# Performance work log

Hardware: AMD Instinct MI355X
Metric: run time of the kernel (lower is better)

The kernel has to match this reference:

```python
import jax, jax.numpy as jnp
import numpy as np

BN_EPSILON = 1e-05


def hard_sigmoid(x):
    return jnp.clip((x + 1.0) / 2.0, 0.0, 1.0)


def setup_inputs() -> dict:
    key = jax.random.key(0)
    kx, kw, kb = jax.random.split(key, 3)
    # NHWC activations
    x = jax.random.normal(kx, (64, 112, 112, 64), dtype=jnp.float32)
    # HWIO kernel initialized ~ truncated_normal(stddev=0.2), then Bernoulli-binarized
    # to +/-1 once at graph-construction time (set_input_shape), so we sample here.
    k_init = 0.2 * jax.random.normal(kw, (3, 3, 64, 64), dtype=jnp.float32)
    kernels = 2.0 * jax.random.bernoulli(kb, hard_sigmoid(k_init)).astype(jnp.float32) - 1.0
    # tf.contrib.layers.batch_norm defaults: center=True (beta), scale=False (no gamma)
    beta = jnp.zeros((64,), dtype=jnp.float32)
    return {"x": x, "kernels": kernels, "beta": beta}


def reference(x, kernels, beta):
    # Training-mode batch norm: per-batch moments over (N, H, W)
    mean = jnp.mean(x, axis=(0, 1, 2))
    var = jnp.var(x, axis=(0, 1, 2))
    x_bn = (x - mean) * jax.lax.rsqrt(var + BN_EPSILON) + beta
    # NOTE: original code computes conv(sign(x_bn), k) but immediately overwrites it
    # with conv(x_bn, k); the effective forward uses the batch-normed (non-signed)
    # activations with the binarized (+/-1) kernels.
    a = jax.lax.conv_general_dilated(
        x_bn, kernels,
        window_strides=(1, 1),
        padding="SAME",
        dimension_numbers=("NHWC", "HWIO", "NHWC"),
    )
    return a
```

## Files before the change

kernel.cpp:

```cpp
#include <hip/hip_runtime.h>

typedef __attribute__((ext_vector_type(8))) short bf16x8;
typedef __attribute__((ext_vector_type(8))) unsigned short u16x8;
typedef __attribute__((ext_vector_type(4))) float f32x4;

#define HW      112
#define CH      64
#define PIX_IMG (HW*HW)
#define N4TOT   (64*112*112*64/4)
#define NPIX_F  802816.0f

#define WS_HV_BYTE  1280
#define WS_W_BYTE   4096
#define WS_XBF_BYTE (4u<<20)

__device__ __forceinline__ unsigned short f2bf(float f) {
  unsigned u = __float_as_uint(f);
  u += 0x7FFFu + ((u >> 16) & 1u);
  return (unsigned short)(u >> 16);
}

__global__ void zero_ws(float* __restrict__ ws) {
  ws[threadIdx.x] = 0.0f;
}

template <bool WRITE_BF>
__global__ __launch_bounds__(256) void stats_kernel(const float* __restrict__ x,
                                                    float* __restrict__ ws,
                                                    unsigned short* __restrict__ xbf) {
  __shared__ float red[128];
  const int tid = threadIdx.x;
  if (tid < 128) red[tid] = 0.0f;
  __syncthreads();

  const float4* __restrict__ x4 = (const float4*)x;
  float4 s = make_float4(0.f, 0.f, 0.f, 0.f);
  float4 q = make_float4(0.f, 0.f, 0.f, 0.f);
  const int stride = gridDim.x * 256;
  #pragma unroll 4
  for (int i = blockIdx.x * 256 + tid; i < N4TOT; i += stride) {
    float4 v = x4[i];
    s.x += v.x; s.y += v.y; s.z += v.z; s.w += v.w;
    q.x = fmaf(v.x, v.x, q.x); q.y = fmaf(v.y, v.y, q.y);
    q.z = fmaf(v.z, v.z, q.z); q.w = fmaf(v.w, v.w, q.w);
    if (WRITE_BF) {
      ushort4 o;
      o.x = f2bf(v.x); o.y = f2bf(v.y); o.z = f2bf(v.z); o.w = f2bf(v.w);
      *(ushort4*)(xbf + 4 * i) = o;
    }
  }
  #pragma unroll
  for (int m = 16; m <= 32; m <<= 1) {
    s.x += __shfl_xor(s.x, m); s.y += __shfl_xor(s.y, m);
    s.z += __shfl_xor(s.z, m); s.w += __shfl_xor(s.w, m);
    q.x += __shfl_xor(q.x, m); q.y += __shfl_xor(q.y, m);
    q.z += __shfl_xor(q.z, m); q.w += __shfl_xor(q.w, m);
  }
  if ((tid & 63) < 16) {
    const int c0 = (tid & 15) * 4;
    atomicAdd(&red[c0 + 0], s.x); atomicAdd(&red[c0 + 1], s.y);
    atomicAdd(&red[c0 + 2], s.z); atomicAdd(&red[c0 + 3], s.w);
    atomicAdd(&red[64 + c0 + 0], q.x); atomicAdd(&red[64 + c0 + 1], q.y);
    atomicAdd(&red[64 + c0 + 2], q.z); atomicAdd(&red[64 + c0 + 3], q.w);
  }
  __syncthreads();
  if (tid < 128) atomicAdd(&ws[tid], red[tid]);
}

__global__ __launch_bounds__(256) void finalize_kernel(const float* __restrict__ beta,
                                                       const float* __restrict__ k,
                                                       float* __restrict__ ws) {
  __shared__ float sb[64];
  __shared__ float part[256];
  const int tid = threadIdx.x;
  if (tid < 64) {
    float mean = ws[tid] * (1.0f / NPIX_F);
    float var  = fmaxf(ws[64 + tid] * (1.0f / NPIX_F) - mean * mean, 0.0f);
    float sc = rsqrtf(var + 1e-5f);
    float b  = beta[tid] - mean * sc;
    ws[128 + tid] = sc;
    ws[192 + tid] = b;
    ((unsigned short*)((char*)ws + WS_HV_BYTE))[tid] = f2bf(-b / sc);
    sb[tid] = b;
  }
  __syncthreads();
  const int co = tid & 63, pt = tid >> 6;
  float a = 0.f;
  #pragma unroll 8
  for (int t = pt; t < 576; t += 4)
    a = fmaf(sb[t & 63], k[t * 64 + co], a);
  part[tid] = a;
  __syncthreads();
  if (tid < 64)
    ws[256 + tid] = part[tid] + part[64 + tid] + part[128 + tid] + part[192 + tid];
}

__global__ __launch_bounds__(256) void prep_w(const float* __restrict__ k,
                                              const float* __restrict__ ws,
                                              unsigned short* __restrict__ wsw) {
  const int oidx = blockIdx.x * 256 + threadIdx.x;
  const int j  = oidx & 7;
  const int co = (oidx >> 3) & 63;
  const int qd = (oidx >> 9) & 3;
  const int t2 = oidx >> 11;
  const int tap = t2 % 9;
  const int h   = t2 / 9;
  const int ci  = h * 32 + qd * 8 + j;
  wsw[oidx] = f2bf(k[(tap * 64 + ci) * 64 + co] * ws[128 + ci]);
}

template <bool USE_BF>
__global__ __launch_bounds__(448, 4) void conv_kernel(const float* __restrict__ x,
                                                      const unsigned short* __restrict__ xbf,
                                                      const unsigned short* __restrict__ wsw,
                                                      const float* __restrict__ ws,
                                                      float* __restrict__ out) {
  __shared__ unsigned short Xs[6 * 114 * 40];
  __shared__ unsigned short Wd[2 * 6144];
  const int tid = threadIdx.x;
  const int bid = blockIdx.x;
  const int n  = bid / 28;
  const int h0 = (bid % 28) * 4;

  const int lane = tid & 63;
  const int wv   = tid >> 6;
  const int qd   = lane >> 4;
  const int cc   = lane & 15;
  const int wvb  = wv * 16;

  const unsigned short* hv = (const unsigned short*)((const char*)ws + WS_HV_BYTE);

  f32x4 acc[4][4];
  {
    const float* bo = ws + 256;
    #pragma unroll
    for (int mt = 0; mt < 4; ++mt) {
      const f32x4 bv = *(const f32x4*)(bo + mt * 16 + qd * 4);
      #pragma unroll
      for (int r = 0; r < 4; ++r) acc[r][mt] = bv;
    }
  }

  for (int half = 0; half < 2; ++half) {
    {
      u16x8 hv8[4];
      #pragma unroll
      for (int o = 0; o < 4; ++o) hv8[o] = *(const u16x8*)(hv + half * 32 + o * 8);
      for (int c = tid; c < 2736; c += 448) {
        const int o  = c & 3;
        const int pi = c >> 2;
        const int p  = pi % 114;
        const int r  = pi / 114;
        const int w  = p - 1;
        const int g  = h0 + r - 1;
        u16x8 v;
        if ((unsigned)w < 112u && (unsigned)g < 112u) {
          const int base = ((n * 112 + g) * 112 + w) * 64 + half * 32 + o * 8;
          if (USE_BF) {
            v = *(const u16x8*)(xbf + base);
          } else {
            const float* sp = x + base;
            const float4 a = *(const float4*)sp;
            const float4 b = *(const float4*)(sp + 4);
            v = (u16x8){f2bf(a.x), f2bf(a.y), f2bf(a.z), f2bf(a.w),
                        f2bf(b.x), f2bf(b.y), f2bf(b.z), f2bf(b.w)};
          }
        } else {
          v = hv8[o];
        }
        *(u16x8*)(&Xs[pi * 40 + o * 8]) = v;
      }
    }
    const unsigned short* wh = wsw + half * 18432;
    for (int t = tid; t < 768; t += 448)
      *(u16x8*)(&Wd[t * 8]) = *(const u16x8*)(wh + t * 8);
    __syncthreads();

    for (int dh = 0; dh < 3; ++dh) {
      if (dh < 2) {
        const unsigned short* ws_src = wh + (dh + 1) * 6144;
        const int nb = ((dh + 1) & 1) * 6144;
        for (int t = tid; t < 768; t += 448)
          *(u16x8*)(&Wd[nb + t * 8]) = *(const u16x8*)(ws_src + t * 8);
      }
      const int cb = (dh & 1) * 6144;
      #pragma unroll
      for (int dw = 0; dw < 3; ++dw) {
        bf16x8 xb[4];
        #pragma unroll
        for (int r = 0; r < 4; ++r)
          xb[r] = *(const bf16x8*)(&Xs[((r + dh) * 114 + wvb + dw + cc) * 40 + qd * 8]);
        #pragma unroll
        for (int mt = 0; mt < 4; ++mt) {
          const bf16x8 wa = *(const bf16x8*)(&Wd[cb + ((dw * 4 + qd) * 64 + mt * 16 + cc) * 8]);
          #pragma unroll
          for (int r = 0; r < 4; ++r)
            acc[r][mt] = __builtin_amdgcn_mfma_f32_16x16x32_bf16(wa, xb[r], acc[r][mt], 0, 0, 0);
        }
      }
      __syncthreads();
    }
  }

  #pragma unroll
  for (int r = 0; r < 4; ++r) {
    const int pix = n * PIX_IMG + (h0 + r) * 112 + wvb + cc;
    float* op = out + pix * 64 + qd * 4;
    #pragma unroll
    for (int mt = 0; mt < 4; ++mt)
      *(f32x4*)(op + mt * 16) = acc[r][mt];
  }
}

extern "C" void kernel_launch(void* const* d_in, const int* in_sizes, int n_in,
                              void* d_out, int out_size, void* d_ws, size_t ws_size,
                              hipStream_t stream) {
  const float* x    = (const float*)d_in[0];
  const float* kern = (const float*)d_in[1];
  const float* beta = (const float*)d_in[2];
  float* out = (float*)d_out;
  float* ws  = (float*)d_ws;
  unsigned short* wsw = (unsigned short*)((char*)d_ws + WS_W_BYTE);
  unsigned short* xbf = (unsigned short*)((char*)d_ws + WS_XBF_BYTE);

  const bool use_bf = ws_size >= (size_t)WS_XBF_BYTE + 102760448ull;

  zero_ws<<<1, 128, 0, stream>>>(ws);
  if (use_bf) stats_kernel<true ><<<1024, 256, 0, stream>>>(x, ws, xbf);
  else        stats_kernel<false><<<1024, 256, 0, stream>>>(x, ws, xbf);
  finalize_kernel<<<1, 256, 0, stream>>>(beta, kern, ws);
  prep_w<<<144, 256, 0, stream>>>(kern, ws, wsw);
  if (use_bf) conv_kernel<true ><<<64 * 28, 448, 0, stream>>>(x, xbf, wsw, ws, out);
  else        conv_kernel<false><<<64 * 28, 448, 0, stream>>>(x, xbf, wsw, ws, out);
}
```

Measured before the change: 485.5 us.

## Restructure conv staging: full-weight LDS, reordered tap loops, block swizzle, nontemporal IO

The conv kernel now loads all nine taps of weights for a half into LDS at once, removing per-row weight double-buffering and two barriers per half. It swaps the loop order to dw-outer/dh-inner with a rotating register window of input rows, which cuts LDS reads. It changes the Xs layout to channel-quad-major and remaps block ids so consecutive blocks spread across XCDs. The stats kernel and output stores now use nontemporal loads and stores. LDS usage grows (about 36KB for weights plus the input tile), which could limit occupancy, and the bf16 staging written nontemporally may not stay cached for the conv pass.

```diff
diff --git a/kernel.cpp b/kernel.cpp
--- a/kernel.cpp
+++ b/kernel.cpp
@@ -2,6 +2,7 @@
 
 typedef __attribute__((ext_vector_type(8))) short bf16x8;
 typedef __attribute__((ext_vector_type(8))) unsigned short u16x8;
+typedef __attribute__((ext_vector_type(4))) unsigned short u16x4;
 typedef __attribute__((ext_vector_type(4))) float f32x4;
 
 #define HW      112
@@ -33,35 +34,35 @@
   if (tid < 128) red[tid] = 0.0f;
   __syncthreads();
 
-  const float4* __restrict__ x4 = (const float4*)x;
-  float4 s = make_float4(0.f, 0.f, 0.f, 0.f);
-  float4 q = make_float4(0.f, 0.f, 0.f, 0.f);
+  const f32x4* __restrict__ x4 = (const f32x4*)x;
+  f32x4 s = {0.f, 0.f, 0.f, 0.f};
+  f32x4 q = {0.f, 0.f, 0.f, 0.f};
   const int stride = gridDim.x * 256;
   #pragma unroll 4
   for (int i = blockIdx.x * 256 + tid; i < N4TOT; i += stride) {
-    float4 v = x4[i];
-    s.x += v.x; s.y += v.y; s.z += v.z; s.w += v.w;
-    q.x = fmaf(v.x, v.x, q.x); q.y = fmaf(v.y, v.y, q.y);
-    q.z = fmaf(v.z, v.z, q.z); q.w = fmaf(v.w, v.w, q.w);
+    f32x4 v = __builtin_nontemporal_load(&x4[i]);
+    s += v;
+    q += v * v;
     if (WRITE_BF) {
-      ushort4 o;
-      o.x = f2bf(v.x); o.y = f2bf(v.y); o.z = f2bf(v.z); o.w = f2bf(v.w);
-      *(ushort4*)(xbf + 4 * i) = o;
+      u16x4 o = {f2bf(v[0]), f2bf(v[1]), f2bf(v[2]), f2bf(v[3])};
+      __builtin_nontemporal_store(o, (u16x4*)(xbf + 4 * i));
     }
   }
   #pragma unroll
   for (int m = 16; m <= 32; m <<= 1) {
-    s.x += __shfl_xor(s.x, m); s.y += __shfl_xor(s.y, m);
-    s.z += __shfl_xor(s.z, m); s.w += __shfl_xor(s.w, m);
-    q.x += __shfl_xor(q.x, m); q.y += __shfl_xor(q.y, m);
-    q.z += __shfl_xor(q.z, m); q.w += __shfl_xor(q.w, m);
+    #pragma unroll
+    for (int j = 0; j < 4; ++j) {
+      s[j] += __shfl_xor(s[j], m);
+      q[j] += __shfl_xor(q[j], m);
+    }
   }
   if ((tid & 63) < 16) {
     const int c0 = (tid & 15) * 4;
-    atomicAdd(&red[c0 + 0], s.x); atomicAdd(&red[c0 + 1], s.y);
-    atomicAdd(&red[c0 + 2], s.z); atomicAdd(&red[c0 + 3], s.w);
-    atomicAdd(&red[64 + c0 + 0], q.x); atomicAdd(&red[64 + c0 + 1], q.y);
-    atomicAdd(&red[64 + c0 + 2], q.z); atomicAdd(&red[64 + c0 + 3], q.w);
+    #pragma unroll
+    for (int j = 0; j < 4; ++j) {
+      atomicAdd(&red[c0 + j], s[j]);
+      atomicAdd(&red[64 + c0 + j], q[j]);
+    }
   }
   __syncthreads();
   if (tid < 128) atomicAdd(&ws[tid], red[tid]);
@@ -115,10 +116,11 @@
                                                       const unsigned short* __restrict__ wsw,
                                                       const float* __restrict__ ws,
                                                       float* __restrict__ out) {
-  __shared__ unsigned short Xs[6 * 114 * 40];
-  __shared__ unsigned short Wd[2 * 6144];
+  __shared__ unsigned short Xs[4 * 6 * 114 * 8];
+  __shared__ unsigned short Wd[2304 * 8];
   const int tid = threadIdx.x;
-  const int bid = blockIdx.x;
+  int bid = (int)blockIdx.x;
+  bid = (bid & 7) * 224 + (bid >> 3);
   const int n  = bid / 28;
   const int h0 = (bid % 28) * 4;
 
@@ -146,7 +148,7 @@
       u16x8 hv8[4];
       #pragma unroll
       for (int o = 0; o < 4; ++o) hv8[o] = *(const u16x8*)(hv + half * 32 + o * 8);
-      for (int c = tid; c < 2736; c += 448) {
+      auto stage = [&](int c) {
         const int o  = c & 3;
         const int pi = c >> 2;
         const int p  = pi % 114;
@@ -160,46 +162,54 @@
             v = *(const u16x8*)(xbf + base);
           } else {
             const float* sp = x + base;
-            const float4 a = *(const float4*)sp;
-            const float4 b = *(const float4*)(sp + 4);
-            v = (u16x8){f2bf(a.x), f2bf(a.y), f2bf(a.z), f2bf(a.w),
-                        f2bf(b.x), f2bf(b.y), f2bf(b.z), f2bf(b.w)};
+            const f32x4 a = *(const f32x4*)sp;
+            const f32x4 b = *(const f32x4*)(sp + 4);
+            v = (u16x8){f2bf(a[0]), f2bf(a[1]), f2bf(a[2]), f2bf(a[3]),
+                        f2bf(b[0]), f2bf(b[1]), f2bf(b[2]), f2bf(b[3])};
           }
         } else {
           v = hv8[o];
         }
-        *(u16x8*)(&Xs[pi * 40 + o * 8]) = v;
-      }
-    }
-    const unsigned short* wh = wsw + half * 18432;
-    for (int t = tid; t < 768; t += 448)
-      *(u16x8*)(&Wd[t * 8]) = *(const u16x8*)(wh + t * 8);
+        *(u16x8*)(&Xs[o * 5472 + pi * 8]) = v;
+      };
+      #pragma unroll
+      for (int kk = 0; kk < 6; ++kk) stage(kk * 448 + tid);
+      if (tid < 48) stage(2688 + tid);
+    }
+    {
+      const unsigned short* wh = wsw + half * 18432;
+      auto wstage = [&](int t) {
+        *(u16x8*)(&Wd[t * 8]) = *(const u16x8*)(wh + t * 8);
+      };
+      #pragma unroll
+      for (int kk = 0; kk < 5; ++kk) wstage(kk * 448 + tid);
+      if (tid < 64) wstage(2240 + tid);
+    }
     __syncthreads();
 
-    for (int dh = 0; dh < 3; ++dh) {
-      if (dh < 2) {
-        const unsigned short* ws_src = wh + (dh + 1) * 6144;
-        const int nb = ((dh + 1) & 1) * 6144;
-        for (int t = tid; t < 768; t += 448)
-          *(u16x8*)(&Wd[nb + t * 8]) = *(const u16x8*)(ws_src + t * 8);
-      }
-      const int cb = (dh & 1) * 6144;
-      #pragma unroll
-      for (int dw = 0; dw < 3; ++dw) {
-        bf16x8 xb[4];
-        #pragma unroll
-        for (int r = 0; r < 4; ++r)
-          xb[r] = *(const bf16x8*)(&Xs[((r + dh) * 114 + wvb + dw + cc) * 40 + qd * 8]);
+    #pragma unroll
+    for (int dw = 0; dw < 3; ++dw) {
+      bf16x8 xb[4];
+      #pragma unroll
+      for (int rr = 0; rr < 4; ++rr)
+        xb[rr] = *(const bf16x8*)(&Xs[qd * 5472 + (rr * 114 + wvb + dw + cc) * 8]);
+      #pragma unroll
+      for (int dh = 0; dh < 3; ++dh) {
+        if (dh)
+          xb[(dh + 3) & 3] =
+              *(const bf16x8*)(&Xs[qd * 5472 + ((dh + 3) * 114 + wvb + dw + cc) * 8]);
         #pragma unroll
         for (int mt = 0; mt < 4; ++mt) {
-          const bf16x8 wa = *(const bf16x8*)(&Wd[cb + ((dw * 4 + qd) * 64 + mt * 16 + cc) * 8]);
+          const bf16x8 wa = *(const bf16x8*)(
+              &Wd[(((dh * 3 + dw) * 4 + qd) * 64 + mt * 16 + cc) * 8]);
           #pragma unroll
           for (int r = 0; r < 4; ++r)
-            acc[r][mt] = __builtin_amdgcn_mfma_f32_16x16x32_bf16(wa, xb[r], acc[r][mt], 0, 0, 0);
+            acc[r][mt] = __builtin_amdgcn_mfma_f32_16x16x32_bf16(wa, xb[(dh + r) & 3],
+                                                                 acc[r][mt], 0, 0, 0);
         }
       }
-      __syncthreads();
-    }
+    }
+    if (half == 0) __syncthreads();
   }
 
   #pragma unroll
@@ -208,7 +218,7 @@
     float* op = out + pix * 64 + qd * 4;
     #pragma unroll
     for (int mt = 0; mt < 4; ++mt)
-      *(f32x4*)(op + mt * 16) = acc[r][mt];
+      __builtin_nontemporal_store(acc[r][mt], (f32x4*)(op + mt * 16));
   }
 }
 
```

Result: no change. 485.2 us (-0.1%).
